# Performance work log

Measured on AMD Instinct MI355X. Metric: run time of the kernel, lower is better.

Reference implementation:

```python
import jax, jax.numpy as jnp
import numpy as np

NUM_EMBEDDINGS = 1024
EMBEDDING_DIM = 64
COMMITMENT_COST = 0.25
N_TOKENS = 131072


def setup_inputs() -> dict:
    key = jax.random.key(0)
    k1, k2 = jax.random.split(key)
    inputs = jax.random.normal(k1, (N_TOKENS, EMBEDDING_DIM), dtype=jnp.float32)
    embedding_w = jax.random.normal(k2, (NUM_EMBEDDINGS, EMBEDDING_DIM), dtype=jnp.float32)
    return {"inputs": inputs, "embedding_w": embedding_w}


def reference(inputs, embedding_w):
    distances = (jnp.sum(inputs ** 2, axis=1, keepdims=True)
                 + jnp.sum(embedding_w ** 2, axis=1)
                 - 2.0 * jnp.matmul(inputs, embedding_w.T))
    encoding_indices = jnp.argmin(distances, axis=1)            # [N]
    encodings = jax.nn.one_hot(encoding_indices, NUM_EMBEDDINGS, dtype=inputs.dtype)  # [N, K]
    quantized = jnp.take(embedding_w, encoding_indices, axis=0)  # gather == one_hot @ W

    # commitment loss (quantized is detached in the torch code)
    e_latent_loss = jnp.mean((jax.lax.stop_gradient(quantized) - inputs) ** 2)
    loss = COMMITMENT_COST * e_latent_loss

    # straight-through estimator
    quantized = inputs + jax.lax.stop_gradient(quantized - inputs)

    avg_probs = jnp.mean(encodings, axis=0)                      # [K]
    perplexity = jnp.exp(-jnp.sum(avg_probs * jnp.log(avg_probs + 1e-10)))
    return loss, quantized, perplexity, encodings
```

## Files before the change

### kernel.cpp

```cpp
#include <hip/hip_runtime.h>

#define NTOK     131072
#define KCODES   1024
#define DIM      64
#define TAU_S    8e-4f
#define FLAG_CAP 16384

typedef unsigned short ushort_t;
typedef unsigned int uint_t;
typedef unsigned char uchar_t;
typedef __attribute__((ext_vector_type(8))) short short8;
typedef __attribute__((ext_vector_type(4))) float f32x4;
typedef __attribute__((ext_vector_type(2))) float nf32x2;


#define BAR_LDS() do {                                        \
    asm volatile("s_waitcnt lgkmcnt(0)" ::: "memory");        \
    __builtin_amdgcn_sched_barrier(0);                        \
    __builtin_amdgcn_s_barrier();                             \
    __builtin_amdgcn_sched_barrier(0);                        \
} while (0)

__device__ inline ushort_t f2bf(float f) {
    uint_t u = __float_as_uint(f);
    return (ushort_t)((u + 0x7FFFu + ((u >> 16) & 1u)) >> 16);
}
__device__ inline float bf2f(ushort_t h) { return __uint_as_float(((uint_t)h) << 16); }

__device__ inline void pack8(float4 p, float4 q, short8& h, short8& l) {
    float v[8] = {p.x, p.y, p.z, p.w, q.x, q.y, q.z, q.w};
#pragma unroll
    for (int j = 0; j < 8; ++j) {
        ushort_t hb = f2bf(v[j]);
        float hf = bf2f(hb);
        ushort_t lb = f2bf(v[j] - hf);
        h[j] = (short)hb;
        l[j] = (short)lb;
    }
}

__global__ __launch_bounds__(256) void vq_prep(const float* __restrict__ W,
                                               uchar_t* __restrict__ Wst,
                                               float* __restrict__ wsq,
                                               uint_t* __restrict__ counts,
                                               uint_t* __restrict__ flag_cnt) {
    const int tid = threadIdx.x;
    if (blockIdx.x == 0) {
#pragma unroll
        for (int j = 0; j < 4; ++j) counts[tid * 4 + j] = 0u;
        if (tid == 0) *flag_cnt = 0u;
    }
    const int e = blockIdx.x * 256 + tid;
    const int k = e >> 6, d = e & 63;
    const float w = W[e];
    const ushort_t hb = f2bf(w);
    const float hf = bf2f(hb);
    const ushort_t lb = f2bf(w - hf);
    const int g = k >> 5, c = k & 31, s = d >> 3, p = d & 7;
    const size_t base = (size_t)g * 8192 + (size_t)s * 512
                      + (size_t)(c ^ (s & 3)) * 16 + (size_t)p * 2;
    *(ushort_t*)(Wst + base)        = hb;
    *(ushort_t*)(Wst + base + 4096) = lb;
    float sq = w * w;
#pragma unroll
    for (int off = 32; off >= 1; off >>= 1) sq += __shfl_xor(sq, off, 64);
    if ((tid & 63) == 0) wsq[e >> 6] = sq;
}

__global__ __launch_bounds__(256) void vq_fused(
    const float* __restrict__ X, const uchar_t* __restrict__ Wst,
    const float* __restrict__ wsq_g, const float* __restrict__ W,
    float* __restrict__ out, ushort_t* __restrict__ idx_g,
    uint_t* __restrict__ counts, float* __restrict__ lossA,
    uint_t* __restrict__ flag_cnt, int* __restrict__ flags)
{
    const int tid   = threadIdx.x;
    const int lane  = tid & 63;
    const int wv    = tid >> 6;
    const int col16 = lane & 15;
    const int ks    = lane >> 4;
    const int TB    = blockIdx.x * 64;
    const int WB    = TB + wv * 16;

    __shared__ __align__(16) char sbuf[2][8192];
    __shared__ float s_xsq[4][16];
    __shared__ int   s_idx[64];

    float* enc = out + 2 + (size_t)NTOK * DIM + (size_t)TB * KCODES;

    short8 xh0, xh1, xl0, xl1;
    {
        const float* xr = X + (size_t)(WB + col16) * DIM + ks * 8;
        float4 a0 = *(const float4*)(xr);
        float4 a1 = *(const float4*)(xr + 4);
        float4 a2 = *(const float4*)(xr + 32);
        float4 a3 = *(const float4*)(xr + 36);
        float xsq = a0.x*a0.x + a0.y*a0.y + a0.z*a0.z + a0.w*a0.w
                  + a1.x*a1.x + a1.y*a1.y + a1.z*a1.z + a1.w*a1.w
                  + a2.x*a2.x + a2.y*a2.y + a2.z*a2.z + a2.w*a2.w
                  + a3.x*a3.x + a3.y*a3.y + a3.z*a3.z + a3.w*a3.w;
        xsq += __shfl_xor(xsq, 16, 64);
        xsq += __shfl_xor(xsq, 32, 64);
        if (lane < 16) s_xsq[wv][lane] = xsq;
        pack8(a0, a1, xh0, xl0);
        pack8(a2, a3, xh1, xl1);
    }

    short8 p0, p1;
    {
        const short8* src = (const short8*)(Wst + (size_t)tid * 16);
        p0 = src[0]; p1 = src[256];
        short8* dst = (short8*)(&sbuf[0][tid * 16]);
        dst[0] = p0; dst[256] = p1;
    }
    __syncthreads();

    float m1[4], m2[4]; int i1[4];
#pragma unroll
    for (int r = 0; r < 4; ++r) { m1[r] = -3.4e38f; m2[r] = -3.4e38f; i1[r] = 0; }

    const int rb = ks * 512 + ((col16 ^ ks) * 16);
    const nf32x2 zz = {0.f, 0.f};
    const f32x4 zero4 = {0.f, 0.f, 0.f, 0.f};

    for (int g = 0; g < 32; ++g) {
        const int cb = g * 32;
        const int b  = g & 1;
        const float c0a = -0.5f * wsq_g[cb + col16];
        const float c0b = -0.5f * wsq_g[cb + 16 + col16];
        if (g < 31) {
            const short8* src = (const short8*)(Wst + (size_t)(g + 1) * 8192 + (size_t)tid * 16);
            p0 = src[0]; p1 = src[256];
        }
        {
            float* zp = enc + g * 2048 + tid * 8;
            *(nf32x2*)(zp)     = zz;
            *(nf32x2*)(zp + 2) = zz;
            *(nf32x2*)(zp + 4) = zz;
            *(nf32x2*)(zp + 6) = zz;
        }
        const char* buf = sbuf[b];
#pragma unroll
        for (int j = 0; j < 2; ++j) {
            const int off = rb + j * 256;
            short8 bh0 = *(const short8*)(buf + off);
            short8 bh1 = *(const short8*)(buf + off + 2048);
            short8 bl0 = *(const short8*)(buf + off + 4096);
            short8 bl1 = *(const short8*)(buf + off + 6144);
            const float c0 = j ? c0b : c0a;
            f32x4 aA, aB;
            aA[0] = c0; aA[1] = c0; aA[2] = c0; aA[3] = c0;
            aB = zero4;
            aA = __builtin_amdgcn_mfma_f32_16x16x32_bf16(xh0, bh0, aA, 0, 0, 0);
            aB = __builtin_amdgcn_mfma_f32_16x16x32_bf16(xh1, bh1, aB, 0, 0, 0);
            aA = __builtin_amdgcn_mfma_f32_16x16x32_bf16(xh0, bl0, aA, 0, 0, 0);
            aB = __builtin_amdgcn_mfma_f32_16x16x32_bf16(xh1, bl1, aB, 0, 0, 0);
            aA = __builtin_amdgcn_mfma_f32_16x16x32_bf16(xl0, bh0, aA, 0, 0, 0);
            aB = __builtin_amdgcn_mfma_f32_16x16x32_bf16(xl1, bh1, aB, 0, 0, 0);
            const int cc = cb + j * 16 + col16;
#pragma unroll
            for (int r = 0; r < 4; ++r) {
                float v = aA[r] + aB[r];
                bool gt = v > m1[r];
                m2[r] = __builtin_amdgcn_fmed3f(v, m1[r], m2[r]);
                i1[r] = gt ? cc : i1[r];
                m1[r] = fmaxf(v, m1[r]);
            }
        }
        if (g < 31) {
            short8* dst = (short8*)(&sbuf[b ^ 1][tid * 16]);
            dst[0] = p0; dst[256] = p1;
            BAR_LDS();
        }
    }

#pragma unroll
    for (int mask = 1; mask <= 8; mask <<= 1) {
#pragma unroll
        for (int r = 0; r < 4; ++r) {
            float v1 = __shfl_xor(m1[r], mask, 64);
            int   j1 = __shfl_xor(i1[r], mask, 64);
            float v2 = __shfl_xor(m2[r], mask, 64);
            bool take = (v1 > m1[r]) || (v1 == m1[r] && j1 < i1[r]);
            m2[r] = take ? fmaxf(m1[r], v2) : fmaxf(v1, m2[r]);
            m1[r] = take ? v1 : m1[r];
            i1[r] = take ? j1 : i1[r];
        }
    }

    float lsum = 0.f;
    if (col16 == 0) {
#pragma unroll
        for (int r = 0; r < 4; ++r) {
            const int trow = ks * 4 + r;
            const int tok = WB + trow;
            s_idx[wv * 16 + trow] = i1[r];
            idx_g[tok] = (ushort_t)i1[r];
            atomicAdd(&counts[i1[r]], 1u);
            if (m1[r] - m2[r] < TAU_S) {
                uint_t pos = atomicAdd(flag_cnt, 1u);
                if (pos < FLAG_CAP) flags[pos] = tok;
                else lsum += s_xsq[wv][trow] - 2.f * m1[r];
            } else {
                lsum += s_xsq[wv][trow] - 2.f * m1[r];
            }
        }
    }
    lsum += __shfl_xor(lsum, 16, 64);
    lsum += __shfl_xor(lsum, 32, 64);
    if (lane == 0) lossA[blockIdx.x * 4 + wv] = lsum;
    __syncthreads();

    if (tid < 64)
        enc[(size_t)tid * KCODES + s_idx[tid]] = 1.f;

    for (int i = tid; i < 64 * DIM; i += 256) {
        const int r = i >> 6, c = i & 63;
        out[1 + (size_t)(TB + r) * DIM + c] = W[(size_t)s_idx[r] * DIM + c];
    }
}

__global__ __launch_bounds__(256) void vq_refine(
    const float* __restrict__ X, const float* __restrict__ W,
    float* __restrict__ out, uint_t* __restrict__ counts,
    double* __restrict__ lossB, const uint_t* __restrict__ flag_cnt,
    const int* __restrict__ flags, const ushort_t* __restrict__ idx_g)
{
    const int tid  = threadIdx.x;
    const int lane = tid & 63;
    const int wid  = blockIdx.x * 4 + (tid >> 6);
    uint_t n = *flag_cnt; if (n > FLAG_CAP) n = FLAG_CAP;

    double lcorr = 0.0;
    for (uint_t e = wid; e < n; e += 1024) {
        const int t   = flags[e];
        const int old = idx_g[t];

        float xf[DIM];
        {
            const float4* xr4 = (const float4*)(X + (size_t)t * DIM);
#pragma unroll
            for (int i = 0; i < 16; ++i) {
                float4 v = xr4[i];
                xf[4*i+0] = v.x; xf[4*i+1] = v.y; xf[4*i+2] = v.z; xf[4*i+3] = v.w;
            }
        }

        double best = 1e300; int bi = KCODES;
        for (int k = 0; k < 16; ++k) {
            const int c = (k << 6) + lane;
            const float* wr = W + (size_t)c * DIM;
            double dsum = 0.0;
#pragma unroll
            for (int d = 0; d < DIM; ++d) {
                double diff = (double)xf[d] - (double)wr[d];
                dsum += diff * diff;
            }
            if (dsum < best) { best = dsum; bi = c; }
        }
#pragma unroll
        for (int mask = 1; mask <= 32; mask <<= 1) {
            double db = __shfl_xor(best, mask, 64);
            int    ib = __shfl_xor(bi, mask, 64);
            if (db < best || (db == best && ib < bi)) { best = db; bi = ib; }
        }
        out[1 + (size_t)t * DIM + lane] = W[(size_t)bi * DIM + lane];
        if (lane == 0) {
            lcorr += best;
            if (bi != old) {
                atomicSub(&counts[old], 1u);
                atomicAdd(&counts[bi], 1u);
                float* encp = out + 2 + (size_t)NTOK * DIM + (size_t)t * KCODES;
                encp[old] = 0.f;
                encp[bi]  = 1.f;
            }
        }
    }
    if (lane == 0) lossB[wid] = lcorr;
}

__global__ __launch_bounds__(256) void vq_finalize(
    const uint_t* __restrict__ counts, const float* __restrict__ lossA,
    const double* __restrict__ lossB, float* __restrict__ out)
{
    int tid = threadIdx.x;
    double ls = 0.0;
    for (int i = tid; i < 8192; i += 256) ls += (double)lossA[i];
    for (int i = tid; i < 1024; i += 256) ls += lossB[i];
    float h = 0.f;
    for (int i = tid; i < KCODES; i += 256) {
        float p = (float)counts[i] * (1.0f / (float)NTOK);
        h += p * logf(p + 1e-10f);
    }
    __shared__ double dred[256];
    dred[tid] = ls;
    __syncthreads();
#pragma unroll
    for (int s = 128; s >= 1; s >>= 1) {
        if (tid < s) dred[tid] += dred[tid + s];
        __syncthreads();
    }
    __shared__ float red[4];
#pragma unroll
    for (int off = 32; off >= 1; off >>= 1) h += __shfl_down(h, off, 64);
    if ((tid & 63) == 0) red[tid >> 6] = h;
    __syncthreads();
    if (tid == 0) {
        float ht = red[0] + red[1] + red[2] + red[3];
        out[(size_t)NTOK * DIM + 1] = expf(-ht);
        out[0] = 0.25f * (float)(dred[0] / ((double)NTOK * DIM));
    }
}

extern "C" void kernel_launch(void* const* d_in, const int* in_sizes, int n_in,
                              void* d_out, int out_size, void* d_ws, size_t ws_size,
                              hipStream_t stream) {
    const float* X = (const float*)d_in[0];
    const float* W = (const float*)d_in[1];
    float* out = (float*)d_out;
    uint_t*   counts   = (uint_t*)d_ws;
    uint_t*   flag_cnt = (uint_t*)((char*)d_ws + 4096);
    float*    lossA    = (float*)((char*)d_ws + 4112);
    double*   lossB    = (double*)((char*)d_ws + 36880);
    float*    wsq      = (float*)((char*)d_ws + 45072);
    uchar_t*  Wst      = (uchar_t*)((char*)d_ws + 49408);
    int*      flags    = (int*)((char*)d_ws + 311552);
    ushort_t* idx_g    = (ushort_t*)((char*)d_ws + 377088);

    vq_prep<<<256, 256, 0, stream>>>(W, Wst, wsq, counts, flag_cnt);
    vq_fused<<<NTOK / 64, 256, 0, stream>>>(X, Wst, wsq, W, out, idx_g,
                                            counts, lossA, flag_cnt, flags);
    vq_refine<<<256, 256, 0, stream>>>(X, W, out, counts, lossB,
                                       flag_cnt, flags, idx_g);
    vq_finalize<<<1, 256, 0, stream>>>(counts, lossA, lossB, out);
}
```

Baseline: 204.7 us.

## Add dedicated zero-store wavefront and stage codebook via direct global-to-LDS loads

A fifth wavefront is added to each block that only writes zeros into the one-hot encoding output, stepping through the 32 codebook groups in lockstep with the compute waves' barriers, and then writes the 1.0 entries once indices are known. The compute waves stop storing zeros and load each codebook tile straight into LDS with global_load_lds, so the register staging copies go away. The goal is to take the large encoding write traffic off the MFMA critical path and remove VGPR round trips. In exchange the barrier count must match exactly across wave roles, every barrier now waits on vmcnt, and the larger block may reduce occupancy.

```diff
diff --git a/kernel.cpp b/kernel.cpp
--- a/kernel.cpp
+++ b/kernel.cpp
@@ -14,11 +14,15 @@
 typedef __attribute__((ext_vector_type(2))) float nf32x2;
 
 
-#define BAR_LDS() do {                                        \
-    asm volatile("s_waitcnt lgkmcnt(0)" ::: "memory");        \
-    __builtin_amdgcn_sched_barrier(0);                        \
-    __builtin_amdgcn_s_barrier();                             \
-    __builtin_amdgcn_sched_barrier(0);                        \
+#define GLOAD_LDS(gsrc, ldst) __builtin_amdgcn_global_load_lds(                 \
+    (const __attribute__((address_space(1))) unsigned int*)(gsrc),              \
+    (__attribute__((address_space(3))) unsigned int*)(ldst), 16, 0, 0)
+
+#define BAR_SCAN() do {                                        \
+    asm volatile("s_waitcnt vmcnt(0) lgkmcnt(0)" ::: "memory"); \
+    __builtin_amdgcn_sched_barrier(0);                          \
+    __builtin_amdgcn_s_barrier();                               \
+    __builtin_amdgcn_sched_barrier(0);                          \
 } while (0)
 
 __device__ inline ushort_t f2bf(float f) {
@@ -67,7 +71,7 @@
     if ((tid & 63) == 0) wsq[e >> 6] = sq;
 }
 
-__global__ __launch_bounds__(256) void vq_fused(
+__global__ __launch_bounds__(320) void vq_fused(
     const float* __restrict__ X, const uchar_t* __restrict__ Wst,
     const float* __restrict__ wsq_g, const float* __restrict__ W,
     float* __restrict__ out, ushort_t* __restrict__ idx_g,
@@ -77,16 +81,33 @@
     const int tid   = threadIdx.x;
     const int lane  = tid & 63;
     const int wv    = tid >> 6;
-    const int col16 = lane & 15;
-    const int ks    = lane >> 4;
     const int TB    = blockIdx.x * 64;
-    const int WB    = TB + wv * 16;
 
     __shared__ __align__(16) char sbuf[2][8192];
     __shared__ float s_xsq[4][16];
     __shared__ int   s_idx[64];
 
     float* enc = out + 2 + (size_t)NTOK * DIM + (size_t)TB * KCODES;
+
+    if (wv == 4) {
+        const nf32x2 zz = {0.f, 0.f};
+        __builtin_amdgcn_s_barrier();
+        for (int g = 0; g < 32; ++g) {
+            float* zp = enc + g * 2048 + lane * 2;
+#pragma unroll
+            for (int i = 0; i < 16; ++i)
+                *(nf32x2*)(zp + i * 128) = zz;
+            if (g < 31) __builtin_amdgcn_s_barrier();
+        }
+        __builtin_amdgcn_s_barrier();
+        asm volatile("s_waitcnt vmcnt(0)" ::: "memory");
+        enc[(size_t)lane * KCODES + s_idx[lane]] = 1.f;
+        return;
+    }
+
+    const int col16 = lane & 15;
+    const int ks    = lane >> 4;
+    const int WB    = TB + wv * 16;
 
     short8 xh0, xh1, xl0, xl1;
     {
@@ -106,21 +127,15 @@
         pack8(a2, a3, xh1, xl1);
     }
 
-    short8 p0, p1;
-    {
-        const short8* src = (const short8*)(Wst + (size_t)tid * 16);
-        p0 = src[0]; p1 = src[256];
-        short8* dst = (short8*)(&sbuf[0][tid * 16]);
-        dst[0] = p0; dst[256] = p1;
-    }
-    __syncthreads();
+    GLOAD_LDS(Wst + (size_t)tid * 16,        &sbuf[0][tid * 16]);
+    GLOAD_LDS(Wst + (size_t)tid * 16 + 4096, &sbuf[0][tid * 16 + 4096]);
+    BAR_SCAN();
 
     float m1[4], m2[4]; int i1[4];
 #pragma unroll
     for (int r = 0; r < 4; ++r) { m1[r] = -3.4e38f; m2[r] = -3.4e38f; i1[r] = 0; }
 
     const int rb = ks * 512 + ((col16 ^ ks) * 16);
-    const nf32x2 zz = {0.f, 0.f};
     const f32x4 zero4 = {0.f, 0.f, 0.f, 0.f};
 
     for (int g = 0; g < 32; ++g) {
@@ -129,15 +144,9 @@
         const float c0a = -0.5f * wsq_g[cb + col16];
         const float c0b = -0.5f * wsq_g[cb + 16 + col16];
         if (g < 31) {
-            const short8* src = (const short8*)(Wst + (size_t)(g + 1) * 8192 + (size_t)tid * 16);
-            p0 = src[0]; p1 = src[256];
-        }
-        {
-            float* zp = enc + g * 2048 + tid * 8;
-            *(nf32x2*)(zp)     = zz;
-            *(nf32x2*)(zp + 2) = zz;
-            *(nf32x2*)(zp + 4) = zz;
-            *(nf32x2*)(zp + 6) = zz;
+            const uchar_t* src = Wst + (size_t)(g + 1) * 8192 + (size_t)tid * 16;
+            GLOAD_LDS(src,        &sbuf[b ^ 1][tid * 16]);
+            GLOAD_LDS(src + 4096, &sbuf[b ^ 1][tid * 16 + 4096]);
         }
         const char* buf = sbuf[b];
 #pragma unroll
@@ -167,11 +176,7 @@
                 m1[r] = fmaxf(v, m1[r]);
             }
         }
-        if (g < 31) {
-            short8* dst = (short8*)(&sbuf[b ^ 1][tid * 16]);
-            dst[0] = p0; dst[256] = p1;
-            BAR_LDS();
-        }
+        if (g < 31) BAR_SCAN();
     }
 
 #pragma unroll
@@ -209,10 +214,11 @@
     lsum += __shfl_xor(lsum, 16, 64);
     lsum += __shfl_xor(lsum, 32, 64);
     if (lane == 0) lossA[blockIdx.x * 4 + wv] = lsum;
-    __syncthreads();
-
-    if (tid < 64)
-        enc[(size_t)tid * KCODES + s_idx[tid]] = 1.f;
+
+    asm volatile("s_waitcnt lgkmcnt(0)" ::: "memory");
+    __builtin_amdgcn_sched_barrier(0);
+    __builtin_amdgcn_s_barrier();
+    __builtin_amdgcn_sched_barrier(0);
 
     for (int i = tid; i < 64 * DIM; i += 256) {
         const int r = i >> 6, c = i & 63;
@@ -328,7 +334,7 @@
     ushort_t* idx_g    = (ushort_t*)((char*)d_ws + 377088);
 
     vq_prep<<<256, 256, 0, stream>>>(W, Wst, wsq, counts, flag_cnt);
-    vq_fused<<<NTOK / 64, 256, 0, stream>>>(X, Wst, wsq, W, out, idx_g,
+    vq_fused<<<NTOK / 64, 320, 0, stream>>>(X, Wst, wsq, W, out, idx_g,
                                             counts, lossA, flag_cnt, flags);
     vq_refine<<<256, 256, 0, stream>>>(X, W, out, counts, lossB,
                                        flag_cnt, flags, idx_g);
```

Measured after the change: 225.1 us. 9.9% more time.
